# Optimization experiments

Measured on AMD Instinct MI355X. Metric: run time of the kernel, lower is better.

## Reference

```python
import jax, jax.numpy as jnp
import numpy as np

N = 8192      # nodes per point set
E = 262144    # edges per graph (avg degree 32)
D = 64        # invar_feats_dim_h == out_feats_dim_h
EF = 32       # edge feature dim
NSIG = 15     # len(all_sigmas_dist)
SKIP_H = 0.5
X_INIT = 0.25
SLOPE = 0.01

PNAMES = ['eW1','eb1','eg1','ebt1','eW2','eb2','eg2','ebt2','qW','kW','vW',
          'nW1','nb1','ng1','nbt1','nW2','nb2','ng2','nbt2',
          'cW1','cb1','cg1','cbt1','cW2','cb2']

def _ln(x, g, b):
    m = jnp.mean(x, -1, keepdims=True)
    v = jnp.mean((x - m) ** 2, -1, keepdims=True)
    return (x - m) * jax.lax.rsqrt(v + 1e-5) * g + b

def _lrelu(x):
    return jnp.where(x > 0, x, SLOPE * x)

def setup_inputs() -> dict:
    key = jax.random.key(0)
    ks = jax.random.split(key, 32)
    rn = lambda i, sh, s=1.0: jax.random.normal(ks[i], sh, jnp.float32) * s
    z = lambda sh: jnp.zeros(sh, jnp.float32)
    o = lambda sh: jnp.ones(sh, jnp.float32)
    return dict(
        coords_A=rn(0, (N, 3)), h_feats_A=rn(1, (N, D)),
        orig_feats_A=rn(2, (N, D)), orig_coords_A=rn(3, (N, 3)),
        edge_feats_A=rn(4, (E, EF)),
        coords_B=rn(5, (N, 3)), h_feats_B=rn(6, (N, D)),
        orig_feats_B=rn(7, (N, D)), orig_coords_B=rn(8, (N, 3)),
        edge_feats_B=rn(9, (E, EF)),
        mask=o((N, N)),
        eW1=rn(10, (2 * D + EF + NSIG, D), 0.05), eb1=z((D,)), eg1=o((D,)), ebt1=z((D,)),
        eW2=rn(11, (D, D), 0.05), eb2=z((D,)), eg2=o((D,)), ebt2=z((D,)),
        qW=rn(12, (D, D), 0.05), kW=rn(13, (D, D), 0.05), vW=rn(14, (D, D), 0.05),
        nW1=rn(15, (4 * D, D), 0.05), nb1=z((D,)), ng1=o((D,)), nbt1=z((D,)),
        nW2=rn(16, (D, D), 0.05), nb2=z((D,)), ng2=o((D,)), nbt2=z((D,)),
        cW1=rn(17, (D, D), 0.05), cb1=z((D,)), cg1=o((D,)), cbt1=z((D,)),
        cW2=rn(18, (D, 1), 0.05), cb2=z((1,)),
        src_A=jax.random.randint(ks[19], (E,), 0, N),
        dst_A=jax.random.randint(ks[20], (E,), 0, N),
        src_B=jax.random.randint(ks[21], (E,), 0, N),
        dst_B=jax.random.randint(ks[22], (E,), 0, N),
    )

def _graph_branch(coords, h, efeat, src, dst, p):
    sigmas = 1.5 ** jnp.arange(NSIG, dtype=jnp.float32)
    x_rel = coords[src] - coords[dst]                       # [E,3] u_sub_v
    d2 = jnp.sum(x_rel ** 2, -1, keepdims=True)             # [E,1]
    rbf = jnp.exp(-d2 / sigmas)                             # [E,15]
    inp = jnp.concatenate([h[src], h[dst], efeat, rbf], -1)
    msg = _ln(inp @ p['eW1'] + p['eb1'], p['eg1'], p['ebt1'])
    msg = _ln(_lrelu(msg) @ p['eW2'] + p['eb2'], p['eg2'], p['ebt2'])  # [E,D]
    # per-edge coordinate coefficient
    coef = _ln(msg @ p['cW1'] + p['cb1'], p['cg1'], p['cbt1'])
    coef = _lrelu(coef) @ p['cW2'] + p['cb2']               # [E,1]
    n = coords.shape[0]
    cnt = jnp.clip(jax.ops.segment_sum(jnp.ones((src.shape[0], 1), coords.dtype), dst, num_segments=n), 1.0)
    x_update = jax.ops.segment_sum(x_rel * coef, dst, num_segments=n) / cnt   # mean over in-edges
    aggr_msg = jax.ops.segment_sum(msg, dst, num_segments=n) / cnt
    return x_update, aggr_msg

def _node_update(h, aggr, att, orig_feats, p):
    inp = jnp.concatenate([h, aggr, att, orig_feats], -1)   # node_norm is Identity
    u = _ln(inp @ p['nW1'] + p['nb1'], p['ng1'], p['nbt1'])
    u = _ln(_lrelu(u) @ p['nW2'] + p['nb2'], p['ng2'], p['nbt2'])
    return SKIP_H * u + (1.0 - SKIP_H) * h

def _forward(coords_A, h_feats_A, orig_feats_A, orig_coords_A, edge_feats_A,
             coords_B, h_feats_B, orig_feats_B, orig_coords_B, edge_feats_B,
             mask, p, src_A, dst_A, src_B, dst_B):
    xupA, aggrA = _graph_branch(coords_A, h_feats_A, edge_feats_A, src_A, dst_A, p)
    xupB, aggrB = _graph_branch(coords_B, h_feats_B, edge_feats_B, src_B, dst_B, p)
    # cross attention A <- B (final_h/pre/post crossmsg norms are identity: type 0)
    q = _lrelu(h_feats_A @ p['qW'])
    k = _lrelu(h_feats_B @ p['kW'])
    v = h_feats_B @ p['vW']
    a = mask * (q @ k.T) - 1000.0 * (1.0 - mask)
    attA = jax.nn.softmax(a, axis=-1) @ v                   # [N_A, D]
    attB = 0.0 * attA                                       # source: 0 * cross_attention_A_feat
    x_new_A = X_INIT * orig_coords_A + (1.0 - X_INIT) * coords_A + xupA
    x_new_B = X_INIT * orig_coords_B + (1.0 - X_INIT) * coords_B + xupB
    h_new_A = _node_update(h_feats_A, aggrA, attA, orig_feats_A, p)
    h_new_B = _node_update(h_feats_B, aggrB, attB, orig_feats_B, p)
    return x_new_A, h_new_A, x_new_B, h_new_B

def reference(coords_A, h_feats_A, orig_feats_A, orig_coords_A, edge_feats_A,
              coords_B, h_feats_B, orig_feats_B, orig_coords_B, edge_feats_B,
              mask,
              eW1, eb1, eg1, ebt1, eW2, eb2, eg2, ebt2, qW, kW, vW,
              nW1, nb1, ng1, nbt1, nW2, nb2, ng2, nbt2,
              cW1, cb1, cg1, cbt1, cW2, cb2,
              src_A, dst_A, src_B, dst_B):
    p = dict(eW1=eW1, eb1=eb1, eg1=eg1, ebt1=ebt1, eW2=eW2, eb2=eb2, eg2=eg2, ebt2=ebt2,
             qW=qW, kW=kW, vW=vW,
             nW1=nW1, nb1=nb1, ng1=ng1, nbt1=nbt1, nW2=nW2, nb2=nb2, ng2=ng2, nbt2=nbt2,
             cW1=cW1, cb1=cb1, cg1=cg1, cbt1=cbt1, cW2=cW2, cb2=cb2)
    return _forward(coords_A, h_feats_A, orig_feats_A, orig_coords_A, edge_feats_A,
                    coords_B, h_feats_B, orig_feats_B, orig_coords_B, edge_feats_B,
                    mask, p, src_A, dst_A, src_B, dst_B)
```

## Files before the change

### kernel.cpp

```cpp
#include <hip/hip_runtime.h>
#include <cstdint>
#include <cstddef>


typedef short bf16x8 __attribute__((ext_vector_type(8)));
typedef float floatx4 __attribute__((ext_vector_type(4)));

#define MFMA16(a, b, c) __builtin_amdgcn_mfma_f32_16x16x32_bf16((a), (b), (c), 0, 0, 0)

__device__ __forceinline__ unsigned short f2bf(float f) {
    unsigned int u = __builtin_bit_cast(unsigned int, f);
    u += 0x7fffu + ((u >> 16) & 1u);
    return (unsigned short)(u >> 16);
}
__device__ __forceinline__ float bf2f(unsigned short u) {
    unsigned int x = ((unsigned int)u) << 16;
    return __builtin_bit_cast(float, x);
}
__device__ __forceinline__ bf16x8 cvt8(const float* __restrict__ p) {
    bf16x8 r;
    #pragma unroll
    for (int j = 0; j < 8; j++) r[j] = (short)f2bf(p[j]);
    return r;
}
__device__ __forceinline__ float rowsum16(float x) {
    x += __shfl_xor(x, 1);
    x += __shfl_xor(x, 2);
    x += __shfl_xor(x, 4);
    x += __shfl_xor(x, 8);
    return x;
}
__device__ __forceinline__ float rowmax16(float x) {
    x = fmaxf(x, __shfl_xor(x, 1));
    x = fmaxf(x, __shfl_xor(x, 2));
    x = fmaxf(x, __shfl_xor(x, 4));
    x = fmaxf(x, __shfl_xor(x, 8));
    return x;
}
__device__ __forceinline__ float lrelu(float x) { return x > 0.f ? x : 0.01f * x; }
__device__ __forceinline__ float ln_rstd(float s2, float mean) {
    float var = s2 * 0.015625f - mean * mean;
    return rsqrtf(fmaxf(var, 0.0f) + 1e-5f);
}

__constant__ float INVSIG[16] = {
    1.0f, 0.6666666865f, 0.4444444597f, 0.2962962985f, 0.1975308657f,
    0.1316872428f, 0.0877914950f, 0.0585276633f, 0.0390184447f, 0.0260122959f,
    0.0173415299f, 0.0115610203f, 0.0077073467f, 0.0051382311f, 0.0034254875f, 0.0f};

__global__ void prep_kernel(const float* __restrict__ hA, const float* __restrict__ hB,
                            const float* __restrict__ efA, const float* __restrict__ efB,
                            unsigned short* __restrict__ hbA, unsigned short* __restrict__ hbB,
                            unsigned short* __restrict__ efbA, unsigned short* __restrict__ efbB)
{
    int q = blockIdx.x * 256 + threadIdx.x;
    const float* s; unsigned short* d; int off;
    if (q < 131072)        { s = hA;  d = hbA;  off = q; }
    else if (q < 262144)   { s = hB;  d = hbB;  off = q - 131072; }
    else if (q < 2359296)  { s = efA; d = efbA; off = q - 262144; }
    else                   { s = efB; d = efbB; off = q - 2359296; }
    float4 v = *(const float4*)(s + (size_t)off * 4);
    ushort4 o;
    o.x = f2bf(v.x); o.y = f2bf(v.y); o.z = f2bf(v.z); o.w = f2bf(v.w);
    *(ushort4*)(d + (size_t)off * 4) = o;
}

__global__ void hist_kernel(const int* __restrict__ dstA, const int* __restrict__ dstB,
                            int* __restrict__ histA, int* __restrict__ histB)
{
    int e = blockIdx.x * 256 + threadIdx.x;
    atomicAdd(&histA[dstA[e]], 1);
    atomicAdd(&histB[dstB[e]], 1);
}

__global__ void scan_kernel(const int* __restrict__ histA, const int* __restrict__ histB,
                            int* __restrict__ rowptrA, int* __restrict__ rowptrB)
{
    const int b = blockIdx.x;
    const int* hist = b ? histB : histA;
    int* rowptr = b ? rowptrB : rowptrA;
    __shared__ int part[1024];
    int t = threadIdx.x;
    int v[8]; int s = 0;
    #pragma unroll
    for (int j = 0; j < 8; j++) { v[j] = hist[t * 8 + j]; s += v[j]; }
    part[t] = s;
    __syncthreads();
    for (int off = 1; off < 1024; off <<= 1) {
        int x = part[t];
        int y = (t >= off) ? part[t - off] : 0;
        __syncthreads();
        part[t] = x + y;
        __syncthreads();
    }
    int run = (t > 0) ? part[t - 1] : 0;
    #pragma unroll
    for (int j = 0; j < 8; j++) { rowptr[t * 8 + j] = run; run += v[j]; }
    if (t == 1023) rowptr[8192] = run;
}

__global__ void scatter_kernel(const int* __restrict__ dstA, const int* __restrict__ dstB,
                               const int* __restrict__ rowptrA, const int* __restrict__ rowptrB,
                               int* __restrict__ curA, int* __restrict__ curB,
                               int* __restrict__ posA, int* __restrict__ posB)
{
    int e = blockIdx.x * 256 + threadIdx.x;
    int dA = dstA[e];
    posA[e] = rowptrA[dA] + atomicAdd(&curA[dA], 1);
    int dB = dstB[e];
    posB[e] = rowptrB[dB] + atomicAdd(&curB[dB], 1);
}

__global__ __launch_bounds__(512, 2) void edge_kernel(
    const float* __restrict__ coordsA, const unsigned short* __restrict__ hbA,
    const unsigned short* __restrict__ efbA, const int* __restrict__ srcA,
    const int* __restrict__ dstA, const int* __restrict__ posA,
    const float* __restrict__ coordsB, const unsigned short* __restrict__ hbB,
    const unsigned short* __restrict__ efbB, const int* __restrict__ srcB,
    const int* __restrict__ dstB, const int* __restrict__ posB,
    const float* __restrict__ eW1, const float* __restrict__ eb1,
    const float* __restrict__ eg1, const float* __restrict__ ebt1,
    const float* __restrict__ eW2, const float* __restrict__ eb2,
    const float* __restrict__ eg2, const float* __restrict__ ebt2,
    const float* __restrict__ cW1, const float* __restrict__ cb1,
    const float* __restrict__ cg1, const float* __restrict__ cbt1,
    const float* __restrict__ cW2, const float* __restrict__ cb2,
    unsigned short* __restrict__ msgbufA, unsigned short* __restrict__ msgbufB,
    float* __restrict__ xupA, float* __restrict__ xupB)
{
    __shared__ __attribute__((aligned(16))) short Wt1[64 * 200];
    __shared__ __attribute__((aligned(16))) short Wt2s[64 * 72];
    __shared__ __attribute__((aligned(16))) short Wc1s[64 * 72];
    __shared__ __attribute__((aligned(16))) float pb[644];
    __shared__ __attribute__((aligned(16))) short msgb[8][16 * 72];

    const int tid = threadIdx.x;

    for (int i = tid; i < 64 * 192; i += 512) {
        int n = i / 192, kk = i - n * 192;
        Wt1[n * 200 + kk] = (kk < 175) ? (short)f2bf(eW1[kk * 64 + n]) : (short)0;
    }
    for (int i = tid; i < 4096; i += 512) {
        int n = i >> 6, kk = i & 63;
        Wt2s[n * 72 + kk] = (short)f2bf(eW2[kk * 64 + n]);
        Wc1s[n * 72 + kk] = (short)f2bf(cW1[kk * 64 + n]);
    }
    if (tid < 64) {
        pb[tid]       = eb1[tid];
        pb[64 + tid]  = eg1[tid];
        pb[128 + tid] = ebt1[tid];
        pb[192 + tid] = eb2[tid];
        pb[256 + tid] = eg2[tid];
        pb[320 + tid] = ebt2[tid];
        pb[384 + tid] = cb1[tid];
        pb[448 + tid] = cg1[tid];
        pb[512 + tid] = cbt1[tid];
        pb[576 + tid] = cW2[tid];
    }
    if (tid == 0) pb[640] = cb2[0];
    __syncthreads();

    const int wave = tid >> 6;
    const int lane = tid & 63;
    const int l15 = lane & 15;
    const int g = lane >> 4;

    for (int gi = blockIdx.x * 8 + wave; gi < 32768; gi += 8192) {
        const int br = gi >> 14;
        const float* coords = br ? coordsB : coordsA;
        const unsigned short* hb = br ? hbB : hbA;
        const unsigned short* efb = br ? efbB : efbA;
        const int* src = br ? srcB : srcA;
        const int* dst = br ? dstB : dstA;
        const int* pos = br ? posB : posA;
        unsigned short* msgbuf = br ? msgbufB : msgbufA;
        float* xup = br ? xupB : xupA;

        const int ebase = (gi & 16383) * 16;
        const int e = ebase + l15;
        const int s = src[e];
        const int d0 = dst[e];
        const int slot = pos[e];

        float xr0 = coords[s * 3 + 0] - coords[d0 * 3 + 0];
        float xr1 = coords[s * 3 + 1] - coords[d0 * 3 + 1];
        float xr2 = coords[s * 3 + 2] - coords[d0 * 3 + 2];
        float d2 = xr0 * xr0 + xr1 * xr1 + xr2 * xr2;

        bf16x8 afr[6];
        afr[0] = *(const bf16x8*)(hb + (size_t)s * 64 + 8 * g);
        afr[1] = *(const bf16x8*)(hb + (size_t)s * 64 + 32 + 8 * g);
        afr[2] = *(const bf16x8*)(hb + (size_t)d0 * 64 + 8 * g);
        afr[3] = *(const bf16x8*)(hb + (size_t)d0 * 64 + 32 + 8 * g);
        afr[4] = *(const bf16x8*)(efb + (size_t)e * 32 + 8 * g);
        {
            bf16x8 a5;
            #pragma unroll
            for (int j = 0; j < 8; j++) {
                int idx = 8 * g + j;
                float rv = 0.0f;
                if (g < 2 && idx < 15) rv = __expf(-d2 * INVSIG[idx & 15]);
                a5[j] = (short)f2bf(rv);
            }
            afr[5] = a5;
        }

        floatx4 acc1[4];
        #pragma unroll
        for (int t = 0; t < 4; t++) acc1[t] = (floatx4)0.0f;
        #pragma unroll
        for (int c = 0; c < 6; c++) {
            #pragma unroll
            for (int t = 0; t < 4; t++) {
                bf16x8 b = *(const bf16x8*)(&Wt1[(t * 16 + l15) * 200 + 32 * c + 8 * g]);
                acc1[t] = MFMA16(afr[c], b, acc1[t]);
            }
        }

        float vv[4][4];
        #pragma unroll
        for (int t = 0; t < 4; t++)
            #pragma unroll
            for (int r = 0; r < 4; r++) vv[t][r] = acc1[t][r] + pb[t * 16 + l15];
        #pragma unroll
        for (int r = 0; r < 4; r++) {
            float s1 = vv[0][r] + vv[1][r] + vv[2][r] + vv[3][r];
            float s2 = vv[0][r] * vv[0][r] + vv[1][r] * vv[1][r] + vv[2][r] * vv[2][r] + vv[3][r] * vv[3][r];
            s1 = rowsum16(s1);
            s2 = rowsum16(s2);
            float mean = s1 * 0.015625f;
            float rstd = ln_rstd(s2, mean);
            int rowoff = (4 * g + r) * 72;
            #pragma unroll
            for (int t = 0; t < 4; t++) {
                int colx = t * 16 + l15;
                float x = (vv[t][r] - mean) * rstd * pb[64 + colx] + pb[128 + colx];
                x = lrelu(x);
                msgb[wave][rowoff + colx] = (short)f2bf(x);
            }
        }

        bf16x8 a2[2];
        a2[0] = *(const bf16x8*)(&msgb[wave][l15 * 72 + 8 * g]);
        a2[1] = *(const bf16x8*)(&msgb[wave][l15 * 72 + 32 + 8 * g]);
        floatx4 acc2[4];
        #pragma unroll
        for (int t = 0; t < 4; t++) acc2[t] = (floatx4)0.0f;
        #pragma unroll
        for (int c = 0; c < 2; c++) {
            #pragma unroll
            for (int t = 0; t < 4; t++) {
                bf16x8 b = *(const bf16x8*)(&Wt2s[(t * 16 + l15) * 72 + 32 * c + 8 * g]);
                acc2[t] = MFMA16(a2[c], b, acc2[t]);
            }
        }
        float vm[4][4];
        #pragma unroll
        for (int t = 0; t < 4; t++)
            #pragma unroll
            for (int r = 0; r < 4; r++) vm[t][r] = acc2[t][r] + pb[192 + t * 16 + l15];
        #pragma unroll
        for (int r = 0; r < 4; r++) {
            float s1 = vm[0][r] + vm[1][r] + vm[2][r] + vm[3][r];
            float s2 = vm[0][r] * vm[0][r] + vm[1][r] * vm[1][r] + vm[2][r] * vm[2][r] + vm[3][r] * vm[3][r];
            s1 = rowsum16(s1);
            s2 = rowsum16(s2);
            float mean = s1 * 0.015625f;
            float rstd = ln_rstd(s2, mean);
            #pragma unroll
            for (int t = 0; t < 4; t++) {
                int colx = t * 16 + l15;
                vm[t][r] = (vm[t][r] - mean) * rstd * pb[256 + colx] + pb[320 + colx];
            }
        }
        #pragma unroll
        for (int r = 0; r < 4; r++) {
            int rowoff = (4 * g + r) * 72;
            #pragma unroll
            for (int t = 0; t < 4; t++) msgb[wave][rowoff + t * 16 + l15] = (short)f2bf(vm[t][r]);
        }

        {
            unsigned short* mrow = msgbuf + (size_t)slot * 64;
            *(bf16x8*)(mrow + 8 * g)      = *(const bf16x8*)(&msgb[wave][l15 * 72 + 8 * g]);
            *(bf16x8*)(mrow + 32 + 8 * g) = *(const bf16x8*)(&msgb[wave][l15 * 72 + 32 + 8 * g]);
        }

        bf16x8 a3[2];
        a3[0] = *(const bf16x8*)(&msgb[wave][l15 * 72 + 8 * g]);
        a3[1] = *(const bf16x8*)(&msgb[wave][l15 * 72 + 32 + 8 * g]);
        floatx4 acc3[4];
        #pragma unroll
        for (int t = 0; t < 4; t++) acc3[t] = (floatx4)0.0f;
        #pragma unroll
        for (int c = 0; c < 2; c++) {
            #pragma unroll
            for (int t = 0; t < 4; t++) {
                bf16x8 b = *(const bf16x8*)(&Wc1s[(t * 16 + l15) * 72 + 32 * c + 8 * g]);
                acc3[t] = MFMA16(a3[c], b, acc3[t]);
            }
        }
        float w3[4][4];
        #pragma unroll
        for (int t = 0; t < 4; t++)
            #pragma unroll
            for (int r = 0; r < 4; r++) w3[t][r] = acc3[t][r] + pb[384 + t * 16 + l15];
        float coefr[4];
        #pragma unroll
        for (int r = 0; r < 4; r++) {
            float s1 = w3[0][r] + w3[1][r] + w3[2][r] + w3[3][r];
            float s2 = w3[0][r] * w3[0][r] + w3[1][r] * w3[1][r] + w3[2][r] * w3[2][r] + w3[3][r] * w3[3][r];
            s1 = rowsum16(s1);
            s2 = rowsum16(s2);
            float mean = s1 * 0.015625f;
            float rstd = ln_rstd(s2, mean);
            float p = 0.f;
            #pragma unroll
            for (int t = 0; t < 4; t++) {
                int colx = t * 16 + l15;
                float x = (w3[t][r] - mean) * rstd * pb[448 + colx] + pb[512 + colx];
                x = lrelu(x);
                p += x * pb[576 + colx];
            }
            p = rowsum16(p);
            coefr[r] = p + pb[640];
        }

        int srcl = (l15 >> 2) << 4;
        float v0 = __shfl(coefr[0], srcl);
        float v1 = __shfl(coefr[1], srcl);
        float v2 = __shfl(coefr[2], srcl);
        float v3 = __shfl(coefr[3], srcl);
        int rsel = l15 & 3;
        float cf = (rsel == 0) ? v0 : (rsel == 1) ? v1 : (rsel == 2) ? v2 : v3;

        if (g < 3) {
            float xrg = (g == 0) ? xr0 : (g == 1) ? xr1 : xr2;
            atomicAdd(&xup[(size_t)d0 * 3 + g], xrg * cf);
        }
    }
}

__global__ __launch_bounds__(256, 4) void gather_kernel(
    const int* __restrict__ rowptrA, const int* __restrict__ rowptrB,
    const unsigned short* __restrict__ msgbufA, const unsigned short* __restrict__ msgbufB,
    float* __restrict__ aggrA, float* __restrict__ aggrB)
{
    const int tid = threadIdx.x;
    const int wave = tid >> 6, lane = tid & 63;
    const int nwaves = gridDim.x * 4;
    for (int u = blockIdx.x * 4 + wave; u < 16384; u += nwaves) {
        const int br = u >> 13;
        const int n = u & 8191;
        const int* rowptr = br ? rowptrB : rowptrA;
        const unsigned short* mb = br ? msgbufB : msgbufA;
        float* aggr = br ? aggrB : aggrA;
        int base = rowptr[n];
        int deg = rowptr[n + 1] - base;
        float a[8];
        #pragma unroll
        for (int j = 0; j < 8; j++) a[j] = 0.f;
        int i = 0;
        for (; i + 8 <= deg; i += 8) {
            #pragma unroll
            for (int j = 0; j < 8; j++)
                a[j] += bf2f(mb[(size_t)(base + i + j) * 64 + lane]);
        }
        for (; i < deg; i++) a[0] += bf2f(mb[(size_t)(base + i) * 64 + lane]);
        float t = (a[0] + a[1]) + (a[2] + a[3]) + ((a[4] + a[5]) + (a[6] + a[7]));
        aggr[(size_t)n * 64 + lane] = t / fmaxf((float)deg, 1.0f);
    }
}

__global__ __launch_bounds__(256, 2) void qkv_kernel(
    const unsigned short* __restrict__ hbA, const unsigned short* __restrict__ hbB,
    const float* __restrict__ qW, const float* __restrict__ kW,
    const float* __restrict__ vW,
    unsigned short* __restrict__ qo, unsigned short* __restrict__ ko,
    unsigned short* __restrict__ vTo)
{
    __shared__ __attribute__((aligned(16))) short Wq[64 * 72];
    __shared__ __attribute__((aligned(16))) short Wk[64 * 72];
    __shared__ __attribute__((aligned(16))) short Wv[64 * 72];
    const int tid = threadIdx.x;
    for (int i = tid; i < 4096; i += 256) {
        int n = i >> 6, kk = i & 63;
        Wq[n * 72 + kk] = (short)f2bf(qW[kk * 64 + n]);
        Wk[n * 72 + kk] = (short)f2bf(kW[kk * 64 + n]);
        Wv[n * 72 + kk] = (short)f2bf(vW[kk * 64 + n]);
    }
    __syncthreads();
    const int wave = tid >> 6, lane = tid & 63, l15 = lane & 15, g = lane >> 4;
    const int row0 = blockIdx.x * 64 + wave * 16;
    bf16x8 aA[2], aB[2];
    aA[0] = *(const bf16x8*)(hbA + (size_t)(row0 + l15) * 64 + 8 * g);
    aA[1] = *(const bf16x8*)(hbA + (size_t)(row0 + l15) * 64 + 32 + 8 * g);
    aB[0] = *(const bf16x8*)(hbB + (size_t)(row0 + l15) * 64 + 8 * g);
    aB[1] = *(const bf16x8*)(hbB + (size_t)(row0 + l15) * 64 + 32 + 8 * g);
    floatx4 aq[4], ak4[4], av[4];
    #pragma unroll
    for (int t = 0; t < 4; t++) { aq[t] = (floatx4)0.0f; ak4[t] = (floatx4)0.0f; av[t] = (floatx4)0.0f; }
    #pragma unroll
    for (int c = 0; c < 2; c++) {
        #pragma unroll
        for (int t = 0; t < 4; t++) {
            int wo = (t * 16 + l15) * 72 + 32 * c + 8 * g;
            aq[t] = MFMA16(aA[c], *(const bf16x8*)(&Wq[wo]), aq[t]);
            ak4[t] = MFMA16(aB[c], *(const bf16x8*)(&Wk[wo]), ak4[t]);
            av[t] = MFMA16(aB[c], *(const bf16x8*)(&Wv[wo]), av[t]);
        }
    }
    #pragma unroll
    for (int t = 0; t < 4; t++) {
        #pragma unroll
        for (int r = 0; r < 4; r++) {
            int orow = row0 + 4 * g + r, ocol = t * 16 + l15;
            qo[(size_t)orow * 64 + ocol] = f2bf(lrelu(aq[t][r]));
            ko[(size_t)orow * 64 + ocol] = f2bf(lrelu(ak4[t][r]));
            vTo[(size_t)ocol * 8192 + orow] = f2bf(av[t][r]);
        }
    }
}

__global__ __launch_bounds__(256, 4) void attn_kernel(
    const unsigned short* __restrict__ qb_, const unsigned short* __restrict__ kb_,
    const unsigned short* __restrict__ vT,
    float* __restrict__ Opart, float* __restrict__ ml)
{
    __shared__ __attribute__((aligned(16))) short pbuf[4][16 * 72];
    const int tid = threadIdx.x;
    const int wave = tid >> 6, lane = tid & 63, l15 = lane & 15, g = lane >> 4;
    const int qblock = blockIdx.x >> 3;
    const int split = blockIdx.x & 7;
    const int qrow0 = qblock * 64 + wave * 16;
    const int kbase = split * 1024;
    bf16x8 qf[2];
    qf[0] = *(const bf16x8*)(qb_ + (size_t)(qrow0 + l15) * 64 + 8 * g);
    qf[1] = *(const bf16x8*)(qb_ + (size_t)(qrow0 + l15) * 64 + 32 + 8 * g);
    float m_[4], l_[4];
    floatx4 oacc[4];
    #pragma unroll
    for (int r = 0; r < 4; r++) { m_[r] = -1.0e30f; l_[r] = 0.f; }
    #pragma unroll
    for (int t = 0; t < 4; t++) oacc[t] = (floatx4)0.0f;

    for (int kt = 0; kt < 16; kt++) {
        const int krow0 = kbase + kt * 64;
        floatx4 sacc[4];
        #pragma unroll
        for (int t = 0; t < 4; t++) sacc[t] = (floatx4)0.0f;
        #pragma unroll
        for (int c = 0; c < 2; c++) {
            #pragma unroll
            for (int t = 0; t < 4; t++) {
                bf16x8 b = *(const bf16x8*)(kb_ + (size_t)(krow0 + t * 16 + l15) * 64 + 32 * c + 8 * g);
                sacc[t] = MFMA16(qf[c], b, sacc[t]);
            }
        }
        #pragma unroll
        for (int r = 0; r < 4; r++) {
            float mx = fmaxf(fmaxf(sacc[0][r], sacc[1][r]), fmaxf(sacc[2][r], sacc[3][r]));
            mx = rowmax16(mx);
            float mn = fmaxf(m_[r], mx);
            float sc = __expf(fminf(m_[r] - mn, 0.f));
            float ps = 0.f;
            int rowoff = (4 * g + r) * 72;
            #pragma unroll
            for (int t = 0; t < 4; t++) {
                float p = __expf(fminf(sacc[t][r] - mn, 0.f));
                ps += p;
                pbuf[wave][rowoff + t * 16 + l15] = (short)f2bf(p);
            }
            ps = rowsum16(ps);
            l_[r] = l_[r] * sc + ps;
            m_[r] = mn;
            #pragma unroll
            for (int t = 0; t < 4; t++) oacc[t][r] *= sc;
        }
        bf16x8 pf[2];
        pf[0] = *(const bf16x8*)(&pbuf[wave][l15 * 72 + 8 * g]);
        pf[1] = *(const bf16x8*)(&pbuf[wave][l15 * 72 + 32 + 8 * g]);
        #pragma unroll
        for (int c = 0; c < 2; c++) {
            #pragma unroll
            for (int t = 0; t < 4; t++) {
                bf16x8 b = *(const bf16x8*)(vT + (size_t)(t * 16 + l15) * 8192 + krow0 + 32 * c + 8 * g);
                oacc[t] = MFMA16(pf[c], b, oacc[t]);
            }
        }
    }
    #pragma unroll
    for (int t = 0; t < 4; t++) {
        #pragma unroll
        for (int r = 0; r < 4; r++) {
            int row = qrow0 + 4 * g + r;
            Opart[((size_t)split * 8192 + row) * 64 + t * 16 + l15] = oacc[t][r];
        }
    }
    if (l15 == 0) {
        #pragma unroll
        for (int r = 0; r < 4; r++) {
            int row = qrow0 + 4 * g + r;
            ml[((size_t)split * 8192 + row) * 2 + 0] = m_[r];
            ml[((size_t)split * 8192 + row) * 2 + 1] = l_[r];
        }
    }
}

__global__ void combine_kernel(const float* __restrict__ Opart, const float* __restrict__ ml,
                               unsigned short* __restrict__ attb)
{
    int idx = blockIdx.x * 256 + threadIdx.x;
    int row = idx >> 6, col = idx & 63;
    float mm = -1.0e30f;
    #pragma unroll
    for (int s = 0; s < 8; s++) mm = fmaxf(mm, ml[((size_t)s * 8192 + row) * 2]);
    float l = 0.f, o = 0.f;
    #pragma unroll
    for (int s = 0; s < 8; s++) {
        float w = __expf(ml[((size_t)s * 8192 + row) * 2] - mm);
        l += w * ml[((size_t)s * 8192 + row) * 2 + 1];
        o += w * Opart[((size_t)s * 8192 + row) * 64 + col];
    }
    attb[(size_t)row * 64 + col] = f2bf(o / l);
}

__global__ __launch_bounds__(256, 2) void node_kernel(
    const float* __restrict__ hA, const float* __restrict__ hB,
    const float* __restrict__ origA, const float* __restrict__ origB,
    const unsigned short* __restrict__ attb,
    const float* __restrict__ aggrA, const float* __restrict__ aggrB,
    const float* __restrict__ nW1, const float* __restrict__ nb1,
    const float* __restrict__ ng1, const float* __restrict__ nbt1,
    const float* __restrict__ nW2, const float* __restrict__ nb2,
    const float* __restrict__ ng2, const float* __restrict__ nbt2,
    float* __restrict__ out)
{
    __shared__ __attribute__((aligned(16))) short W1t[64 * 264];
    __shared__ __attribute__((aligned(16))) short W2t[64 * 72];
    __shared__ __attribute__((aligned(16))) float pb[6 * 64];
    __shared__ __attribute__((aligned(16))) short ubuf[4][16 * 72];
    const int tid = threadIdx.x;
    for (int i = tid; i < 64 * 256; i += 256) {
        int n = i >> 8, kk = i & 255;
        W1t[n * 264 + kk] = (short)f2bf(nW1[kk * 64 + n]);
    }
    for (int i = tid; i < 4096; i += 256) {
        int n = i >> 6, kk = i & 63;
        W2t[n * 72 + kk] = (short)f2bf(nW2[kk * 64 + n]);
    }
    if (tid < 64) {
        pb[tid]       = nb1[tid];
        pb[64 + tid]  = ng1[tid];
        pb[128 + tid] = nbt1[tid];
        pb[192 + tid] = nb2[tid];
        pb[256 + tid] = ng2[tid];
        pb[320 + tid] = nbt2[tid];
    }
    __syncthreads();
    const int wave = tid >> 6, lane = tid & 63, l15 = lane & 15, g = lane >> 4;
    const int unit = blockIdx.x * 4 + wave;
    const int br = unit >> 9;
    const int nb_ = (unit & 511) * 16;
    const float* h = br ? hB : hA;
    const float* orig = br ? origB : origA;
    const float* aggr = br ? aggrB : aggrA;
    const size_t outbase = br ? 573440 : 24576;

    const int row = nb_ + l15;

    bf16x8 af[8];
    af[0] = cvt8(h + (size_t)row * 64 + 8 * g);
    af[1] = cvt8(h + (size_t)row * 64 + 32 + 8 * g);
    af[2] = cvt8(aggr + (size_t)row * 64 + 8 * g);
    af[3] = cvt8(aggr + (size_t)row * 64 + 32 + 8 * g);
    if (br == 0) {
        af[4] = *(const bf16x8*)(attb + (size_t)row * 64 + 8 * g);
        af[5] = *(const bf16x8*)(attb + (size_t)row * 64 + 32 + 8 * g);
    } else {
        af[4] = (bf16x8)0;
        af[5] = (bf16x8)0;
    }
    af[6] = cvt8(orig + (size_t)row * 64 + 8 * g);
    af[7] = cvt8(orig + (size_t)row * 64 + 32 + 8 * g);

    floatx4 acc1[4];
    #pragma unroll
    for (int t = 0; t < 4; t++) acc1[t] = (floatx4)0.0f;
    #pragma unroll
    for (int c = 0; c < 8; c++) {
        #pragma unroll
        for (int t = 0; t < 4; t++) {
            bf16x8 b = *(const bf16x8*)(&W1t[(t * 16 + l15) * 264 + 32 * c + 8 * g]);
            acc1[t] = MFMA16(af[c], b, acc1[t]);
        }
    }
    float vv[4][4];
    #pragma unroll
    for (int t = 0; t < 4; t++)
        #pragma unroll
        for (int r = 0; r < 4; r++) vv[t][r] = acc1[t][r] + pb[t * 16 + l15];
    #pragma unroll
    for (int r = 0; r < 4; r++) {
        float s1 = vv[0][r] + vv[1][r] + vv[2][r] + vv[3][r];
        float s2 = vv[0][r] * vv[0][r] + vv[1][r] * vv[1][r] + vv[2][r] * vv[2][r] + vv[3][r] * vv[3][r];
        s1 = rowsum16(s1);
        s2 = rowsum16(s2);
        float mean = s1 * 0.015625f;
        float rstd = ln_rstd(s2, mean);
        int rowoff = (4 * g + r) * 72;
        #pragma unroll
        for (int t = 0; t < 4; t++) {
            int colx = t * 16 + l15;
            float x = (vv[t][r] - mean) * rstd * pb[64 + colx] + pb[128 + colx];
            x = lrelu(x);
            ubuf[wave][rowoff + colx] = (short)f2bf(x);
        }
    }
    bf16x8 a2[2];
    a2[0] = *(const bf16x8*)(&ubuf[wave][l15 * 72 + 8 * g]);
    a2[1] = *(const bf16x8*)(&ubuf[wave][l15 * 72 + 32 + 8 * g]);
    floatx4 acc2[4];
    #pragma unroll
    for (int t = 0; t < 4; t++) acc2[t] = (floatx4)0.0f;
    #pragma unroll
    for (int c = 0; c < 2; c++) {
        #pragma unroll
        for (int t = 0; t < 4; t++) {
            bf16x8 b = *(const bf16x8*)(&W2t[(t * 16 + l15) * 72 + 32 * c + 8 * g]);
            acc2[t] = MFMA16(a2[c], b, acc2[t]);
        }
    }
    float u2[4][4];
    #pragma unroll
    for (int t = 0; t < 4; t++)
        #pragma unroll
        for (int r = 0; r < 4; r++) u2[t][r] = acc2[t][r] + pb[192 + t * 16 + l15];
    #pragma unroll
    for (int r = 0; r < 4; r++) {
        float s1 = u2[0][r] + u2[1][r] + u2[2][r] + u2[3][r];
        float s2 = u2[0][r] * u2[0][r] + u2[1][r] * u2[1][r] + u2[2][r] * u2[2][r] + u2[3][r] * u2[3][r];
        s1 = rowsum16(s1);
        s2 = rowsum16(s2);
        float mean = s1 * 0.015625f;
        float rstd = ln_rstd(s2, mean);
        #pragma unroll
        for (int t = 0; t < 4; t++) {
            int colx = t * 16 + l15;
            float u = (u2[t][r] - mean) * rstd * pb[256 + colx] + pb[320 + colx];
            size_t orow = (size_t)(nb_ + 4 * g + r);
            float hh = h[orow * 64 + colx];
            out[outbase + orow * 64 + colx] = 0.5f * u + 0.5f * hh;
        }
    }
}

__global__ void xnew_kernel(
    const float* __restrict__ coordsA, const float* __restrict__ origcA,
    const float* __restrict__ coordsB, const float* __restrict__ origcB,
    const float* __restrict__ xupA, const float* __restrict__ xupB,
    const int* __restrict__ rowptrA, const int* __restrict__ rowptrB,
    float* __restrict__ out)
{
    int i = blockIdx.x * 256 + threadIdx.x;
    int br = (i >= 24576) ? 1 : 0;
    int j = i - br * 24576;
    const float* coords = br ? coordsB : coordsA;
    const float* origc = br ? origcB : origcA;
    const float* xup = br ? xupB : xupA;
    const int* rp = br ? rowptrB : rowptrA;
    int node = j / 3;
    float cnt = (float)(rp[node + 1] - rp[node]);
    float val = 0.25f * origc[j] + 0.75f * coords[j] + xup[j] / fmaxf(cnt, 1.0f);
    out[(br ? 548864 : 0) + j] = val;
}

extern "C" void kernel_launch(void* const* d_in, const int* in_sizes, int n_in,
                              void* d_out, int out_size, void* d_ws, size_t ws_size,
                              hipStream_t stream)
{
    int base = n_in - 29;
    for (int i = 0; i < n_in; i++) {
        if (in_sizes[i] == 11200) { base = i; break; }
    }
    const float* coordsA = (const float*)d_in[0];
    const float* hA      = (const float*)d_in[1];
    const float* origA   = (const float*)d_in[2];
    const float* origcA  = (const float*)d_in[3];
    const float* efA     = (const float*)d_in[4];
    const float* coordsB = (const float*)d_in[5];
    const float* hB      = (const float*)d_in[6];
    const float* origB   = (const float*)d_in[7];
    const float* origcB  = (const float*)d_in[8];
    const float* efB     = (const float*)d_in[9];
    const float* P[25];
    for (int k = 0; k < 25; k++) P[k] = (const float*)d_in[base + k];
    const int* srcA = (const int*)d_in[base + 25];
    const int* dstA = (const int*)d_in[base + 26];
    const int* srcB = (const int*)d_in[base + 27];
    const int* dstB = (const int*)d_in[base + 28];

    char* ws = (char*)d_ws;
    unsigned short* msgbufA = (unsigned short*)(ws + 0);
    unsigned short* msgbufB = (unsigned short*)(ws + 33554432);
    float* Opart  = (float*)(ws + 0);
    float* mlbuf  = (float*)(ws + 16777216);
    unsigned short* hbA  = (unsigned short*)(ws + 67108864);
    unsigned short* hbB  = (unsigned short*)(ws + 68157440);
    unsigned short* efbA = (unsigned short*)(ws + 69206016);
    unsigned short* efbB = (unsigned short*)(ws + 85983232);
    float* aggrA  = (float*)(ws + 102760448);
    float* aggrB  = (float*)(ws + 104857600);
    unsigned short* qbuf = (unsigned short*)(ws + 106954752);
    unsigned short* kbuf = (unsigned short*)(ws + 108003328);
    unsigned short* vTb  = (unsigned short*)(ws + 109051904);
    unsigned short* attb = (unsigned short*)(ws + 110100480);
    float* xupA = (float*)(ws + 111149056);
    float* xupB = (float*)(ws + 111247360);
    int* histA  = (int*)(ws + 111345664);
    int* histB  = (int*)(ws + 111378432);
    int* curA   = (int*)(ws + 111411200);
    int* curB   = (int*)(ws + 111443968);
    int* rowptrA = (int*)(ws + 111476736);
    int* rowptrB = (int*)(ws + 111517696);
    int* posA   = (int*)(ws + 111558656);
    int* posB   = (int*)(ws + 112607232);
    float* out = (float*)d_out;

    hipMemsetAsync(ws + 111149056, 0, 327680, stream);

    prep_kernel<<<17408, 256, 0, stream>>>(hA, hB, efA, efB, hbA, hbB, efbA, efbB);

    hist_kernel<<<1024, 256, 0, stream>>>(dstA, dstB, histA, histB);
    scan_kernel<<<2, 1024, 0, stream>>>(histA, histB, rowptrA, rowptrB);
    scatter_kernel<<<1024, 256, 0, stream>>>(dstA, dstB, rowptrA, rowptrB,
                                             curA, curB, posA, posB);

    edge_kernel<<<1024, 512, 0, stream>>>(
        coordsA, hbA, efbA, srcA, dstA, posA,
        coordsB, hbB, efbB, srcB, dstB, posB,
        P[0], P[1], P[2], P[3], P[4], P[5], P[6], P[7],
        P[19], P[20], P[21], P[22], P[23], P[24],
        msgbufA, msgbufB, xupA, xupB);

    gather_kernel<<<2048, 256, 0, stream>>>(rowptrA, rowptrB, msgbufA, msgbufB,
                                            aggrA, aggrB);

    qkv_kernel<<<128, 256, 0, stream>>>(hbA, hbB, P[8], P[9], P[10], qbuf, kbuf, vTb);

    attn_kernel<<<1024, 256, 0, stream>>>(qbuf, kbuf, vTb, Opart, mlbuf);
    combine_kernel<<<2048, 256, 0, stream>>>(Opart, mlbuf, attb);

    node_kernel<<<256, 256, 0, stream>>>(
        hA, hB, origA, origB, attb, aggrA, aggrB,
        P[11], P[12], P[13], P[14], P[15], P[16], P[17], P[18], out);

    xnew_kernel<<<192, 256, 0, stream>>>(
        coordsA, origcA, coordsB, origcB, xupA, xupB, rowptrA, rowptrB, out);
}
```

Measured before the change: 393.0 us.

## Move eW1 bf16 transpose to prep kernel and read from global; vectorize gather

Converts and transposes the first edge-MLP weight into a bf16 global buffer once in the prep kernel, instead of each edge block staging it in shared memory. The edge kernel now reads those B fragments straight from global/L2, which shrinks LDS use and raises launch_bounds occupancy from 2 to 4 blocks. The gather kernel now loads 8 rows of 8 bf16 per wave instruction and reduces with shuffles rather than doing scalar per-lane loads. cvt8 also gets vectorized loads. The trade-off is more global-memory traffic for the weights in the inner MFMA loop, plus possible register pressure at the higher occupancy.

```diff
diff --git a/kernel.cpp b/kernel.cpp
--- a/kernel.cpp
+++ b/kernel.cpp
@@ -18,9 +18,13 @@
     return __builtin_bit_cast(float, x);
 }
 __device__ __forceinline__ bf16x8 cvt8(const float* __restrict__ p) {
+    float4 v0 = *(const float4*)(p);
+    float4 v1 = *(const float4*)(p + 4);
     bf16x8 r;
-    #pragma unroll
-    for (int j = 0; j < 8; j++) r[j] = (short)f2bf(p[j]);
+    r[0] = (short)f2bf(v0.x); r[1] = (short)f2bf(v0.y);
+    r[2] = (short)f2bf(v0.z); r[3] = (short)f2bf(v0.w);
+    r[4] = (short)f2bf(v1.x); r[5] = (short)f2bf(v1.y);
+    r[6] = (short)f2bf(v1.z); r[7] = (short)f2bf(v1.w);
     return r;
 }
 __device__ __forceinline__ float rowsum16(float x) {
@@ -50,10 +54,26 @@
 
 __global__ void prep_kernel(const float* __restrict__ hA, const float* __restrict__ hB,
                             const float* __restrict__ efA, const float* __restrict__ efB,
+                            const float* __restrict__ eW1,
                             unsigned short* __restrict__ hbA, unsigned short* __restrict__ hbB,
-                            unsigned short* __restrict__ efbA, unsigned short* __restrict__ efbB)
+                            unsigned short* __restrict__ efbA, unsigned short* __restrict__ efbB,
+                            unsigned short* __restrict__ w1g)
 {
     int q = blockIdx.x * 256 + threadIdx.x;
+    if (q >= 4456448) {
+        int qq = q - 4456448;
+        int i0 = qq * 4;
+        ushort4 o;
+        #pragma unroll
+        for (int j = 0; j < 4; j++) {
+            int i = i0 + j;
+            int n = i / 192, k = i - n * 192;
+            float val = (k < 175) ? eW1[k * 64 + n] : 0.0f;
+            ((unsigned short*)&o)[j] = f2bf(val);
+        }
+        *(ushort4*)(w1g + i0) = o;
+        return;
+    }
     const float* s; unsigned short* d; int off;
     if (q < 131072)        { s = hA;  d = hbA;  off = q; }
     else if (q < 262144)   { s = hB;  d = hbB;  off = q - 131072; }
@@ -111,14 +131,15 @@
     posB[e] = rowptrB[dB] + atomicAdd(&curB[dB], 1);
 }
 
-__global__ __launch_bounds__(512, 2) void edge_kernel(
+__global__ __launch_bounds__(512, 4) void edge_kernel(
     const float* __restrict__ coordsA, const unsigned short* __restrict__ hbA,
     const unsigned short* __restrict__ efbA, const int* __restrict__ srcA,
     const int* __restrict__ dstA, const int* __restrict__ posA,
     const float* __restrict__ coordsB, const unsigned short* __restrict__ hbB,
     const unsigned short* __restrict__ efbB, const int* __restrict__ srcB,
     const int* __restrict__ dstB, const int* __restrict__ posB,
-    const float* __restrict__ eW1, const float* __restrict__ eb1,
+    const unsigned short* __restrict__ W1g,
+    const float* __restrict__ eb1,
     const float* __restrict__ eg1, const float* __restrict__ ebt1,
     const float* __restrict__ eW2, const float* __restrict__ eb2,
     const float* __restrict__ eg2, const float* __restrict__ ebt2,
@@ -128,7 +149,6 @@
     unsigned short* __restrict__ msgbufA, unsigned short* __restrict__ msgbufB,
     float* __restrict__ xupA, float* __restrict__ xupB)
 {
-    __shared__ __attribute__((aligned(16))) short Wt1[64 * 200];
     __shared__ __attribute__((aligned(16))) short Wt2s[64 * 72];
     __shared__ __attribute__((aligned(16))) short Wc1s[64 * 72];
     __shared__ __attribute__((aligned(16))) float pb[644];
@@ -136,10 +156,6 @@
 
     const int tid = threadIdx.x;
 
-    for (int i = tid; i < 64 * 192; i += 512) {
-        int n = i / 192, kk = i - n * 192;
-        Wt1[n * 200 + kk] = (kk < 175) ? (short)f2bf(eW1[kk * 64 + n]) : (short)0;
-    }
     for (int i = tid; i < 4096; i += 512) {
         int n = i >> 6, kk = i & 63;
         Wt2s[n * 72 + kk] = (short)f2bf(eW2[kk * 64 + n]);
@@ -165,6 +181,8 @@
     const int l15 = lane & 15;
     const int g = lane >> 4;
 
+    const unsigned short* W1base = W1g + (size_t)l15 * 192 + 8 * g;
+
     for (int gi = blockIdx.x * 8 + wave; gi < 32768; gi += 8192) {
         const int br = gi >> 14;
         const float* coords = br ? coordsB : coordsA;
@@ -212,7 +230,7 @@
         for (int c = 0; c < 6; c++) {
             #pragma unroll
             for (int t = 0; t < 4; t++) {
-                bf16x8 b = *(const bf16x8*)(&Wt1[(t * 16 + l15) * 200 + 32 * c + 8 * g]);
+                bf16x8 b = *(const bf16x8*)(W1base + (size_t)t * 16 * 192 + 32 * c);
                 acc1[t] = MFMA16(afr[c], b, acc1[t]);
             }
         }
@@ -280,15 +298,15 @@
             for (int t = 0; t < 4; t++) msgb[wave][rowoff + t * 16 + l15] = (short)f2bf(vm[t][r]);
         }
 
-        {
-            unsigned short* mrow = msgbuf + (size_t)slot * 64;
-            *(bf16x8*)(mrow + 8 * g)      = *(const bf16x8*)(&msgb[wave][l15 * 72 + 8 * g]);
-            *(bf16x8*)(mrow + 32 + 8 * g) = *(const bf16x8*)(&msgb[wave][l15 * 72 + 32 + 8 * g]);
-        }
-
         bf16x8 a3[2];
         a3[0] = *(const bf16x8*)(&msgb[wave][l15 * 72 + 8 * g]);
         a3[1] = *(const bf16x8*)(&msgb[wave][l15 * 72 + 32 + 8 * g]);
+        {
+            unsigned short* mrow = msgbuf + (size_t)slot * 64;
+            *(bf16x8*)(mrow + 8 * g)      = a3[0];
+            *(bf16x8*)(mrow + 32 + 8 * g) = a3[1];
+        }
+
         floatx4 acc3[4];
         #pragma unroll
         for (int t = 0; t < 4; t++) acc3[t] = (floatx4)0.0f;
@@ -348,6 +366,7 @@
 {
     const int tid = threadIdx.x;
     const int wave = tid >> 6, lane = tid & 63;
+    const int r8 = lane >> 3, c8 = lane & 7;
     const int nwaves = gridDim.x * 4;
     for (int u = blockIdx.x * 4 + wave; u < 16384; u += nwaves) {
         const int br = u >> 13;
@@ -362,13 +381,29 @@
         for (int j = 0; j < 8; j++) a[j] = 0.f;
         int i = 0;
         for (; i + 8 <= deg; i += 8) {
-            #pragma unroll
-            for (int j = 0; j < 8; j++)
-                a[j] += bf2f(mb[(size_t)(base + i + j) * 64 + lane]);
-        }
-        for (; i < deg; i++) a[0] += bf2f(mb[(size_t)(base + i) * 64 + lane]);
-        float t = (a[0] + a[1]) + (a[2] + a[3]) + ((a[4] + a[5]) + (a[6] + a[7]));
-        aggr[(size_t)n * 64 + lane] = t / fmaxf((float)deg, 1.0f);
+            bf16x8 v = *(const bf16x8*)(mb + (size_t)(base + i + r8) * 64 + c8 * 8);
+            #pragma unroll
+            for (int j = 0; j < 8; j++) a[j] += bf2f((unsigned short)v[j]);
+        }
+        int rem = deg - i;
+        if (r8 < rem) {
+            bf16x8 v = *(const bf16x8*)(mb + (size_t)(base + i + r8) * 64 + c8 * 8);
+            #pragma unroll
+            for (int j = 0; j < 8; j++) a[j] += bf2f((unsigned short)v[j]);
+        }
+        #pragma unroll
+        for (int j = 0; j < 8; j++) {
+            a[j] += __shfl_xor(a[j], 8);
+            a[j] += __shfl_xor(a[j], 16);
+            a[j] += __shfl_xor(a[j], 32);
+        }
+        if (r8 == 0) {
+            float inv = 1.0f / fmaxf((float)deg, 1.0f);
+            float4 w0 = make_float4(a[0] * inv, a[1] * inv, a[2] * inv, a[3] * inv);
+            float4 w1 = make_float4(a[4] * inv, a[5] * inv, a[6] * inv, a[7] * inv);
+            *(float4*)(aggr + (size_t)n * 64 + c8 * 8) = w0;
+            *(float4*)(aggr + (size_t)n * 64 + c8 * 8 + 4) = w1;
+        }
     }
 }
 
@@ -725,11 +760,13 @@
     int* rowptrB = (int*)(ws + 111517696);
     int* posA   = (int*)(ws + 111558656);
     int* posB   = (int*)(ws + 112607232);
+    unsigned short* w1g = (unsigned short*)(ws + 113655808);
     float* out = (float*)d_out;
 
     hipMemsetAsync(ws + 111149056, 0, 327680, stream);
 
-    prep_kernel<<<17408, 256, 0, stream>>>(hA, hB, efA, efB, hbA, hbB, efbA, efbB);
+    prep_kernel<<<17420, 256, 0, stream>>>(hA, hB, efA, efB, P[0],
+                                           hbA, hbB, efbA, efbB, w1g);
 
     hist_kernel<<<1024, 256, 0, stream>>>(dstA, dstB, histA, histB);
     scan_kernel<<<2, 1024, 0, stream>>>(histA, histB, rowptrA, rowptrB);
@@ -739,7 +776,8 @@
     edge_kernel<<<1024, 512, 0, stream>>>(
         coordsA, hbA, efbA, srcA, dstA, posA,
         coordsB, hbB, efbB, srcB, dstB, posB,
-        P[0], P[1], P[2], P[3], P[4], P[5], P[6], P[7],
+        w1g,
+        P[1], P[2], P[3], P[4], P[5], P[6], P[7],
         P[19], P[20], P[21], P[22], P[23], P[24],
         msgbufA, msgbufB, xupA, xupB);
 
```

New measurement: 452.1 us. +15.0%, slower.
